# Kernel tuning notes

Hardware: AMD Instinct MI355X
Metric: run time of the kernel (lower is better)

Reference implementation:

```python
import jax, jax.numpy as jnp
import numpy as np
from jax import lax

B, C_IN, H, W = 4, 1536, 24, 24
MID, DIM = 768, 384
HEADS = 8; DIM_HEAD = 48; GROUPS = 8
DS = 3; OFF_SCALE = 4.0; OFF_K = 3
CPB_DIM = DIM // 4  # 96


def conv1x1(x, w):
    # x: (B,Cin,H,W), w: (Cout,Cin)
    return jnp.einsum('bchw,oc->bohw', x, w)


def grouped_conv1x1(x, w):
    # x: (B,G*Ci,H,W), w: (G,Co,Ci)  == torch Conv2d(groups=G, k=1, bias=False)
    b, c, h, ww = x.shape
    g, co, ci = w.shape
    return jnp.einsum('bgihw,goi->bgohw', x.reshape(b, g, ci, h, ww), w).reshape(b, g * co, h, ww)


def grid_sample_bilinear(img, grid):
    # torch F.grid_sample: bilinear, padding_mode='zeros', align_corners=False
    # img (N,C,H,W); grid (N,Ho,Wo,2) with [...,0]=x, [...,1]=y in [-1,1]
    n, c, h, w = img.shape
    x = ((grid[..., 0] + 1.0) * w - 1.0) * 0.5
    y = ((grid[..., 1] + 1.0) * h - 1.0) * 0.5
    x0 = jnp.floor(x); y0 = jnp.floor(y)
    wx = x - x0; wy = y - y0
    x0 = x0.astype(jnp.int32); y0 = y0.astype(jnp.int32)
    img_nhwc = jnp.transpose(img, (0, 2, 3, 1))
    bidx = jnp.arange(n)[:, None, None]

    def tap(ix, iy, wgt):
        valid = (ix >= 0) & (ix < w) & (iy >= 0) & (iy < h)
        v = img_nhwc[bidx, jnp.clip(iy, 0, h - 1), jnp.clip(ix, 0, w - 1)]  # (N,Ho,Wo,C)
        return v * (wgt * valid)[..., None]

    out = (tap(x0, y0, (1 - wx) * (1 - wy)) + tap(x0 + 1, y0, wx * (1 - wy))
           + tap(x0, y0 + 1, (1 - wx) * wy) + tap(x0 + 1, y0 + 1, wx * wy))
    return jnp.transpose(out, (0, 3, 1, 2))


def xy_grid(h, w, dtype):
    # create_grid_like: channel0 = x (width coord), channel1 = y (height coord)
    gx, gy = jnp.meshgrid(jnp.arange(w, dtype=dtype), jnp.arange(h, dtype=dtype), indexing='xy')
    return gx, gy


def normalize_pair(g0, g1, h, w):
    # faithful to lucidrains normalize_grid: channel0 scaled by (h-1), channel1 by (w-1)
    g0 = 2.0 * g0 / max(h - 1, 1) - 1.0
    g1 = 2.0 * g1 / max(w - 1, 1) - 1.0
    return jnp.stack([g0, g1], axis=-1)


def deform_attn(x, Wq, Wk, Wv, Wdw, bdw, Wpw, cw1, cb1, cw2, cb2, cw3, cb3, Wout, bout):
    b, c, h, w = x.shape
    q = grouped_conv1x1(x, Wq)                                 # (b,384,h,w)
    gq = q.reshape(b * GROUPS, c // GROUPS, h, w)
    # to_offsets: depthwise conv k=3 stride=3 pad=0 -> GELU -> 1x1 (->2) -> tanh -> *offset_scale
    off = lax.conv_general_dilated(gq, Wdw, (DS, DS), 'VALID',
                                   dimension_numbers=('NCHW', 'OIHW', 'NCHW'),
                                   feature_group_count=c // GROUPS) + bdw[None, :, None, None]
    off = jax.nn.gelu(off, approximate=False)
    off = jnp.tanh(jnp.einsum('bchw,oc->bohw', off, Wpw)) * OFF_SCALE   # (b*g,2,hp,wp)
    hp, wp = off.shape[-2], off.shape[-1]
    gx, gy = xy_grid(hp, wp, x.dtype)
    vgrid_scaled = normalize_pair(gx + off[:, 0], gy + off[:, 1], hp, wp)  # (b*g,hp,wp,2)
    kv = grid_sample_bilinear(x.reshape(b * GROUPS, c // GROUPS, h, w), vgrid_scaled)
    kv = kv.reshape(b, c, hp, wp)
    k = grouped_conv1x1(kv, Wk); v = grouped_conv1x1(kv, Wv)
    q = q * (DIM_HEAD ** -0.5)
    sh = lambda t: t.reshape(t.shape[0], HEADS, DIM_HEAD, -1).transpose(0, 1, 3, 2)
    qh, kh, vh = sh(q), sh(k), sh(v)                            # (b,H,i,d),(b,H,j,d)
    sim = jnp.einsum('bhid,bhjd->bhij', qh, kh)
    # CPB relative position bias
    qx, qy = xy_grid(h, w, x.dtype)
    grid_q = normalize_pair(qx, qy, h, w).reshape(1, h * w, 2)
    grid_kv = vgrid_scaled.reshape(b * GROUPS, hp * wp, 2)
    pos = grid_q[:, :, None, :] - grid_kv[:, None, :, :]        # (b*g,i,j,2)
    bias = jnp.sign(pos) * jnp.log1p(jnp.abs(pos))
    bias = jax.nn.relu(bias @ cw1.T + cb1)
    bias = jax.nn.relu(bias @ cw2.T + cb2)
    bias = (bias @ cw3.T + cb3).reshape(b, GROUPS, h * w, hp * wp)  # heads//offset_groups == 1
    attn = jax.nn.softmax(sim + bias, axis=-1)
    out = jnp.einsum('bhij,bhjd->bhid', attn, vh)
    out = out.transpose(0, 1, 3, 2).reshape(b, HEADS * DIM_HEAD, h, w)
    return conv1x1(out, Wout) + bout[None, :, None, None]


def setup_inputs() -> dict:
    key = jax.random.key(0)
    ks = jax.random.split(key, 20)
    s = 0.02
    p = lambda i, shape: jax.random.normal(ks[i], shape, jnp.float32) * s
    return {
        'x': jax.random.normal(ks[0], (B, C_IN, H, W), jnp.float32),
        'W1': p(1, (MID, C_IN)), 'W2': p(2, (DIM, MID)),
        'W3': p(3, (MID, DIM)), 'W4': p(4, (C_IN, MID)),
        'Wq': p(5, (GROUPS, DIM // GROUPS, DIM // GROUPS)),
        'Wk': p(6, (GROUPS, DIM // GROUPS, DIM // GROUPS)),
        'Wv': p(7, (GROUPS, DIM // GROUPS, DIM // GROUPS)),
        'Wdw': p(8, (DIM // GROUPS, 1, OFF_K, OFF_K)), 'bdw': p(9, (DIM // GROUPS,)),
        'Wpw': p(10, (2, DIM // GROUPS)),
        'cpb_w1': p(11, (CPB_DIM, 2)), 'cpb_b1': p(12, (CPB_DIM,)),
        'cpb_w2': p(13, (CPB_DIM, CPB_DIM)), 'cpb_b2': p(14, (CPB_DIM,)),
        'cpb_w3': p(15, (1, CPB_DIM)), 'cpb_b3': p(16, (1,)),
        'Wout': p(17, (DIM, DIM)), 'bout': p(18, (DIM,)),
    }


def reference(x, W1, W2, W3, W4, Wq, Wk, Wv, Wdw, bdw, Wpw,
              cpb_w1, cpb_b1, cpb_w2, cpb_b2, cpb_w3, cpb_b3, Wout, bout):
    h = jax.nn.relu(conv1x1(x, W1))
    h = jax.nn.relu(conv1x1(h, W2))
    h = jax.nn.relu(deform_attn(h, Wq, Wk, Wv, Wdw, bdw, Wpw,
                                cpb_w1, cpb_b1, cpb_w2, cpb_b2, cpb_w3, cpb_b3, Wout, bout))
    h = jax.nn.relu(conv1x1(h, W3))
    return jax.nn.relu(conv1x1(h, W4) + x)
```

## Files before the change

### kernel.cpp

```cpp
#include <hip/hip_runtime.h>

typedef float        fx4 __attribute__((ext_vector_type(4)));
typedef float        fx2 __attribute__((ext_vector_type(2)));
typedef unsigned int ux4 __attribute__((ext_vector_type(4)));
typedef short        bf8 __attribute__((ext_vector_type(8)));

#define DEVI static __device__ __forceinline__

DEVI unsigned f2bf1(float f) {
  union { float f; unsigned u; } v; v.f = f;
  return (v.u + 0x7FFFu + ((v.u >> 16) & 1u)) >> 16;
}
DEVI float bf2f(unsigned h) {
  union { unsigned u; float f; } v; v.u = h << 16; return v.f;
}
DEVI unsigned cvtpk(float lo, float hi) {
  unsigned r;
  asm("v_cvt_pk_bf16_f32 %0, %1, %2" : "=v"(r) : "v"(lo), "v"(hi));
  return r;
}
DEVI void unp8(ux4 u, float* o) {
  o[0] = bf2f(u[0] & 0xffffu); o[1] = bf2f(u[0] >> 16);
  o[2] = bf2f(u[1] & 0xffffu); o[3] = bf2f(u[1] >> 16);
  o[4] = bf2f(u[2] & 0xffffu); o[5] = bf2f(u[2] >> 16);
  o[6] = bf2f(u[3] & 0xffffu); o[7] = bf2f(u[3] >> 16);
}
DEVI void gload16(const void* g, void* l) {
  __builtin_amdgcn_global_load_lds(
      (const __attribute__((address_space(1))) unsigned*)(uintptr_t)(g),
      (__attribute__((address_space(3))) unsigned*)(unsigned)(uintptr_t)(l),
      16, 0, 0);
}
#define DPP_ADD(v, ctrl)                                                      \
  do {                                                                        \
    union { float f; int i; } _s, _d;                                         \
    _s.f = (v);                                                               \
    _d.i = __builtin_amdgcn_update_dpp(0, _s.i, (ctrl), 0xf, 0xf, false);     \
    (v) += _d.f;                                                              \
  } while (0)
DEVI float dpp_sum16(float v) {
  DPP_ADD(v, 0xB1);
  DPP_ADD(v, 0x4E);
  DPP_ADD(v, 0x124);
  DPP_ADD(v, 0x128);
  return v;
}

#define TABLO (-1.6f)
#define TABD  (3.2f / 255.f)
#define TABDI (255.f / 3.2f)

__global__ __launch_bounds__(256) void k_wconv(const float* __restrict__ W1,
                                               const float* __restrict__ W2,
                                               const float* __restrict__ W3,
                                               const float* __restrict__ W4,
                                               const float* __restrict__ Wout,
                                               const float* __restrict__ cw2,
                                               const float* __restrict__ Wq,
                                               unsigned* __restrict__ dst,
                                               unsigned* __restrict__ Wqd) {
  const size_t p = (size_t)blockIdx.x * 256 + threadIdx.x;
  if (p < 1552896) {
    const float* s; size_t base;
    if (p < 589824)       { s = W1;   base = 0; }
    else if (p < 737280)  { s = W2;   base = 589824; }
    else if (p < 884736)  { s = W3;   base = 737280; }
    else if (p < 1474560) { s = W4;   base = 884736; }
    else if (p < 1548288) { s = Wout; base = 1474560; }
    else                  { s = cw2;  base = 1548288; }
    const size_t lp = p - base;
    dst[p] = cvtpk(s[lp * 2], s[lp * 2 + 1]);
  } else if (p < 1626624) {
    const int q = (int)(p - 1552896);
    const int o = q / 192, cp = q % 192;
    const int c0 = cp * 2, c1 = c0 + 1;
    const int g = o / 48, lr = o % 48;
    const int lo = g * 48, hi = lo + 48;
    const float f0 = (c0 >= lo && c0 < hi) ? Wq[((size_t)g * 48 + lr) * 48 + (c0 - lo)] : 0.f;
    const float f1 = (c1 >= lo && c1 < hi) ? Wq[((size_t)g * 48 + lr) * 48 + (c1 - lo)] : 0.f;
    Wqd[q] = cvtpk(f0, f1);
  }
}

__global__ __launch_bounds__(256) void k_transpose(const float* __restrict__ x,
                                                   unsigned short* __restrict__ xT) {
  __shared__ float tile[64][65];
  const int t = threadIdx.x;
  const int b = blockIdx.z, c0 = blockIdx.x * 64, p0 = blockIdx.y * 64;
  const int tl = t & 63, th = t >> 6;
#pragma unroll
  for (int r = 0; r < 16; ++r) {
    int c = th * 16 + r;
    tile[c][tl] = x[((size_t)b * 1536 + c0 + c) * 576 + p0 + tl];
  }
  __syncthreads();
#pragma unroll
  for (int r = 0; r < 16; ++r) {
    int p = th * 16 + r;
    xT[((size_t)b * 576 + p0 + p) * 1536 + c0 + tl] = (unsigned short)f2bf1(tile[tl][p]);
  }
}

#define ROWOF(q) ((((q) >> 7) << 4) + ((q) & 15))
#define KOF(q)   (((((q) >> 6) & 1) << 5) + ((((q) >> 4) & 3) << 3))
template<int BN, bool BIASADD, bool FINAL, bool RELU>
__global__ __launch_bounds__(256, 4) void k_gemm(const unsigned short* __restrict__ A,
                                                 const unsigned short* __restrict__ Wb,
                                                 const float* __restrict__ bias,
                                                 const float* __restrict__ resid,
                                                 void* __restrict__ outp, int K, int M) {
  constexpr int BCH = BN / 32;
  constexpr int NJT = BN / 32;
  __shared__ __align__(16) unsigned short As[3][4096];
  __shared__ __align__(16) unsigned short Bs[3][BN * 64];
  const int t = threadIdx.x;
  const int bz = blockIdx.z, j0 = blockIdx.x * BN, i0 = blockIdx.y * 64;
  const int lane = t & 63, wid = t >> 6;
  const int wi = wid >> 1, wj = wid & 1;
  const int lrow = lane & 15, g4 = lane >> 4;

  const unsigned short* pa0 = A + ((size_t)(bz * 576 + i0 + ROWOF(t))) * K + KOF(t);
  const unsigned short* pa1 = A + ((size_t)(bz * 576 + i0 + ROWOF(t + 256))) * K + KOF(t + 256);
  const unsigned short* pb[BCH];
#pragma unroll
  for (int c = 0; c < BCH; ++c) {
    const int q = t + c * 256;
    pb[c] = Wb + ((size_t)(j0 + ROWOF(q))) * K + KOF(q);
  }
  auto stage = [&](int buf, int ko) {
    gload16(pa0 + ko, &As[buf][t * 8]);
    gload16(pa1 + ko, &As[buf][(t + 256) * 8]);
#pragma unroll
    for (int c = 0; c < BCH; ++c) gload16(pb[c] + ko, &Bs[buf][(t + c * 256) * 8]);
  };
  fx4 acc[2][NJT] = {};
  const int nk = K >> 6;
  stage(0, 0);
  if (nk > 1) stage(1, 64);
  int cur = 0;
  for (int ki = 0; ki < nk; ++ki) {
    if (ki + 1 < nk) {
      if constexpr (BCH == 2) asm volatile("s_waitcnt vmcnt(4)" ::: "memory");
      else                    asm volatile("s_waitcnt vmcnt(6)" ::: "memory");
    } else {
      asm volatile("s_waitcnt vmcnt(0)" ::: "memory");
    }
    __builtin_amdgcn_s_barrier();
    __builtin_amdgcn_sched_barrier(0);
    asm volatile("" ::: "memory");
    if (ki + 2 < nk) {
      int b2 = cur - 1; if (b2 < 0) b2 = 2;
      stage(b2, (ki + 2) * 64);
    }
    const unsigned short* ab = &As[cur][0];
    const unsigned short* bb = &Bs[cur][0];
#pragma unroll
    for (int kk = 0; kk < 2; ++kk) {
      bf8 a0 = *(const bf8*)(ab + (((wi * 2 + 0) * 2 + kk) * 64 + lane) * 8);
      bf8 a1 = *(const bf8*)(ab + (((wi * 2 + 1) * 2 + kk) * 64 + lane) * 8);
#pragma unroll
      for (int jt = 0; jt < NJT; ++jt) {
        bf8 b = *(const bf8*)(bb + (((wj * NJT + jt) * 2 + kk) * 64 + lane) * 8);
        acc[0][jt] = __builtin_amdgcn_mfma_f32_16x16x32_bf16(a0, b, acc[0][jt], 0, 0, 0);
        acc[1][jt] = __builtin_amdgcn_mfma_f32_16x16x32_bf16(a1, b, acc[1][jt], 0, 0, 0);
      }
    }
    cur = (cur == 2) ? 0 : cur + 1;
  }
#pragma unroll
  for (int it = 0; it < 2; ++it) {
    const int row0 = i0 + wi * 32 + it * 16 + g4 * 4;
#pragma unroll
    for (int jt = 0; jt < NJT; ++jt) {
      fx4 v = acc[it][jt];
      const int m = j0 + wj * (BN / 2) + jt * 16 + lrow;
      if (BIASADD) {
        float bv = bias[m];
        v[0] += bv; v[1] += bv; v[2] += bv; v[3] += bv;
      }
      if (FINAL) {
        const fx4 xr = *(const fx4*)(resid + ((size_t)bz * M + m) * 576 + row0);
        fx4 ov;
        ov[0] = fmaxf(v[0] + xr[0], 0.f); ov[1] = fmaxf(v[1] + xr[1], 0.f);
        ov[2] = fmaxf(v[2] + xr[2], 0.f); ov[3] = fmaxf(v[3] + xr[3], 0.f);
        *(fx4*)((float*)outp + ((size_t)bz * M + m) * 576 + row0) = ov;
      } else {
        unsigned short* o = (unsigned short*)outp;
#pragma unroll
        for (int r = 0; r < 4; ++r) {
          const float ov = RELU ? fmaxf(v[r], 0.f) : v[r];
          o[((size_t)(bz * 576) + row0 + r) * M + m] = (unsigned short)f2bf1(ov);
        }
      }
    }
  }
}
#undef ROWOF
#undef KOF

__global__ __launch_bounds__(256, 2) void k_sample(const unsigned short* __restrict__ qT,
                                                   const unsigned short* __restrict__ h2T,
                                                   const float* __restrict__ Wdw,
                                                   const float* __restrict__ bdw,
                                                   const float* __restrict__ Wpw,
                                                   const float* __restrict__ Wk,
                                                   const float* __restrict__ Wv,
                                                   float* __restrict__ vgrid,
                                                   float* __restrict__ kT,
                                                   float* __restrict__ vT) {
  __shared__ float vg[32];
  __shared__ __align__(16) unsigned short kvls[768];
  const int blk = blockIdx.x;
  const int bg = blk >> 2, pg = blk & 3;
  const int b = bg >> 3, g = bg & 7;
  const int t = threadIdx.x;
  const int pl = t >> 4;
  const int cq = t & 15;
  const int pos = pg * 16 + pl;
  const int oy = pos >> 3, ox = pos & 7;
  const int ch0 = cq * 3;
  float s0 = bdw[ch0], s1 = bdw[ch0 + 1], s2 = bdw[ch0 + 2];
#pragma unroll
  for (int ky = 0; ky < 3; ++ky) {
#pragma unroll
    for (int kx = 0; kx < 3; ++kx) {
      const unsigned short* rp =
          qT + ((size_t)b * 576 + (oy * 3 + ky) * 24 + ox * 3 + kx) * 384 + g * 48 + ch0;
      const int tap = ky * 3 + kx;
      s0 = fmaf(bf2f(rp[0]), Wdw[(ch0 + 0) * 9 + tap], s0);
      s1 = fmaf(bf2f(rp[1]), Wdw[(ch0 + 1) * 9 + tap], s1);
      s2 = fmaf(bf2f(rp[2]), Wdw[(ch0 + 2) * 9 + tap], s2);
    }
  }
  float a0 = 0.f, a1 = 0.f;
  {
    const float z0 = s0, z1 = s1, z2 = s2;
    const float g0 = 0.5f * z0 * (1.f + erff(z0 * 0.70710678118654752f));
    const float g1 = 0.5f * z1 * (1.f + erff(z1 * 0.70710678118654752f));
    const float g2 = 0.5f * z2 * (1.f + erff(z2 * 0.70710678118654752f));
    a0 = g0 * Wpw[ch0] + g1 * Wpw[ch0 + 1] + g2 * Wpw[ch0 + 2];
    a1 = g0 * Wpw[48 + ch0] + g1 * Wpw[48 + ch0 + 1] + g2 * Wpw[48 + ch0 + 2];
  }
  a0 = dpp_sum16(a0);
  a1 = dpp_sum16(a1);
  const float gx = ((float)ox + tanhf(a0) * 4.f) * (2.f / 7.f) - 1.f;
  const float gy = ((float)oy + tanhf(a1) * 4.f) * (2.f / 7.f) - 1.f;
  if (cq == 0) {
    vg[pl * 2 + 0] = gx; vg[pl * 2 + 1] = gy;
    vgrid[bg * 128 + pos * 2 + 0] = gx;
    vgrid[bg * 128 + pos * 2 + 1] = gy;
  }
  __syncthreads();
  {
    const float nx = vg[pl * 2 + 0], ny = vg[pl * 2 + 1];
    const float xs = ((nx + 1.f) * 24.f - 1.f) * 0.5f;
    const float ys = ((ny + 1.f) * 24.f - 1.f) * 0.5f;
    const float x0f = floorf(xs), y0f = floorf(ys);
    const float wx = xs - x0f, wy = ys - y0f;
    const int x0 = (int)x0f, y0 = (int)y0f;
    float c0a = 0.f, c1a = 0.f, c2a = 0.f;
    const float tw[4] = {(1.f - wx) * (1.f - wy), wx * (1.f - wy), (1.f - wx) * wy, wx * wy};
    const int tx[4] = {x0, x0 + 1, x0, x0 + 1};
    const int ty[4] = {y0, y0, y0 + 1, y0 + 1};
#pragma unroll
    for (int tp = 0; tp < 4; ++tp) {
      const int ix = tx[tp], iy = ty[tp];
      const float w = tw[tp] * ((ix >= 0 && ix < 24 && iy >= 0 && iy < 24) ? 1.f : 0.f);
      const int cx = min(max(ix, 0), 23), cy = min(max(iy, 0), 23);
      const unsigned short* rp = h2T + ((size_t)b * 576 + cy * 24 + cx) * 384 + g * 48 + ch0;
      c0a = fmaf(bf2f(rp[0]), w, c0a);
      c1a = fmaf(bf2f(rp[1]), w, c1a);
      c2a = fmaf(bf2f(rp[2]), w, c2a);
    }
    kvls[pl * 48 + ch0 + 0] = (unsigned short)f2bf1(c0a);
    kvls[pl * 48 + ch0 + 1] = (unsigned short)f2bf1(c1a);
    kvls[pl * 48 + ch0 + 2] = (unsigned short)f2bf1(c2a);
  }
  __syncthreads();
#pragma unroll
  for (int r = 0; r < 3; ++r) {
    const int idx = t + r * 256;
    const int j = idx / 48, o = idx % 48;
    const unsigned short* rp = &kvls[j * 48];
    const float* wkp = Wk + ((size_t)g * 48 + o) * 48;
    const float* wvp = Wv + ((size_t)g * 48 + o) * 48;
    float ak = 0.f, av = 0.f;
#pragma unroll
    for (int c8 = 0; c8 < 6; ++c8) {
      ux4 u = *(const ux4*)(rp + c8 * 8);
      float va[8]; unp8(u, va);
      fx4 wk0 = *(const fx4*)(wkp + c8 * 8); fx4 wk1 = *(const fx4*)(wkp + c8 * 8 + 4);
      fx4 wv0 = *(const fx4*)(wvp + c8 * 8); fx4 wv1 = *(const fx4*)(wvp + c8 * 8 + 4);
#pragma unroll
      for (int e = 0; e < 4; ++e) {
        ak = fmaf(va[e], wk0[e], ak); ak = fmaf(va[4 + e], wk1[e], ak);
        av = fmaf(va[e], wv0[e], av); av = fmaf(va[4 + e], wv1[e], av);
      }
    }
    kT[(size_t)bg * 3072 + (pg * 16 + j) * 48 + o] = ak;
    vT[(size_t)bg * 3072 + (pg * 16 + j) * 48 + o] = av;
  }
}

__global__ __launch_bounds__(256) void k_cpb_tab(const float* __restrict__ cw1,
                                                 const float* __restrict__ cb1,
                                                 const unsigned short* __restrict__ cw2b,
                                                 const float* __restrict__ cb2,
                                                 const float* __restrict__ cw3,
                                                 const float* __restrict__ cb3,
                                                 float* __restrict__ Tb) {
  __shared__ __align__(16) unsigned short Ws[1152 * 8];
  __shared__ __align__(16) float Cs[288];
  const int t = threadIdx.x;
  const int wid = t >> 6, lane = t & 63;
  const int lrow = lane & 15, g16 = lane >> 4;
#pragma unroll
  for (int rep = 0; rep < 5; ++rep) {
    const int q = t + rep * 256;
    if (q < 1152) {
      const int s = q >> 6, l = q & 63;
      const int jt = s / 3, kk = s - jt * 3;
      const int n = jt * 16 + (l & 15);
      const int k = kk * 32 + ((l >> 4) & 3) * 8;
      gload16(cw2b + (size_t)n * 96 + k, &Ws[q * 8]);
    }
  }
  for (int q = t; q < 288; q += 256) Cs[q] = (q < 192) ? cw1[q] : cb1[q - 192];
  float cb2v[6], cw3v[6];
#pragma unroll
  for (int jt = 0; jt < 6; ++jt) {
    cb2v[jt] = cb2[jt * 16 + lrow];
    cw3v[jt] = cw3[jt * 16 + lrow];
  }
  const float cb3v = cb3[0];
  __syncthreads();
  const int base = blockIdx.x * 256 + wid * 64;
  float uu[4], vv[4];
#pragma unroll
  for (int mt = 0; mt < 4; ++mt) {
    const int e = base + mt * 16 + lrow;
    uu[mt] = TABLO + TABD * (float)(e >> 8);
    vv[mt] = TABLO + TABD * (float)(e & 255);
  }
  bf8 afr[4][3];
#pragma unroll
  for (int kk = 0; kk < 3; ++kk) {
    const int kb = kk * 32 + g16 * 8;
    fx4 w0 = *(const fx4*)&Cs[kb * 2];
    fx4 w1 = *(const fx4*)&Cs[kb * 2 + 4];
    fx4 w2 = *(const fx4*)&Cs[kb * 2 + 8];
    fx4 w3 = *(const fx4*)&Cs[kb * 2 + 12];
    fx4 b0 = *(const fx4*)&Cs[192 + kb];
    fx4 b1 = *(const fx4*)&Cs[192 + kb + 4];
#pragma unroll
    for (int mt = 0; mt < 4; ++mt) {
      float h[8];
      h[0] = fmaxf(fmaf(w0[0], uu[mt], fmaf(w0[1], vv[mt], b0[0])), 0.f);
      h[1] = fmaxf(fmaf(w0[2], uu[mt], fmaf(w0[3], vv[mt], b0[1])), 0.f);
      h[2] = fmaxf(fmaf(w1[0], uu[mt], fmaf(w1[1], vv[mt], b0[2])), 0.f);
      h[3] = fmaxf(fmaf(w1[2], uu[mt], fmaf(w1[3], vv[mt], b0[3])), 0.f);
      h[4] = fmaxf(fmaf(w2[0], uu[mt], fmaf(w2[1], vv[mt], b1[0])), 0.f);
      h[5] = fmaxf(fmaf(w2[2], uu[mt], fmaf(w2[3], vv[mt], b1[1])), 0.f);
      h[6] = fmaxf(fmaf(w3[0], uu[mt], fmaf(w3[1], vv[mt], b1[2])), 0.f);
      h[7] = fmaxf(fmaf(w3[2], uu[mt], fmaf(w3[3], vv[mt], b1[3])), 0.f);
      ux4 pk;
      pk[0] = cvtpk(h[0], h[1]); pk[1] = cvtpk(h[2], h[3]);
      pk[2] = cvtpk(h[4], h[5]); pk[3] = cvtpk(h[6], h[7]);
      afr[mt][kk] = *(bf8*)&pk;
    }
  }
  fx4 part[4] = {};
#pragma unroll
  for (int jt = 0; jt < 6; ++jt) {
    bf8 bf0 = *(const bf8*)&Ws[((jt * 3 + 0) * 64 + lane) * 8];
    bf8 bf1 = *(const bf8*)&Ws[((jt * 3 + 1) * 64 + lane) * 8];
    bf8 bf2 = *(const bf8*)&Ws[((jt * 3 + 2) * 64 + lane) * 8];
#pragma unroll
    for (int mt = 0; mt < 4; ++mt) {
      fx4 acc = {cb2v[jt], cb2v[jt], cb2v[jt], cb2v[jt]};
      acc = __builtin_amdgcn_mfma_f32_16x16x32_bf16(afr[mt][0], bf0, acc, 0, 0, 0);
      acc = __builtin_amdgcn_mfma_f32_16x16x32_bf16(afr[mt][1], bf1, acc, 0, 0, 0);
      acc = __builtin_amdgcn_mfma_f32_16x16x32_bf16(afr[mt][2], bf2, acc, 0, 0, 0);
#pragma unroll
      for (int r = 0; r < 4; ++r)
        part[mt][r] = fmaf(fmaxf(acc[r], 0.f), cw3v[jt], part[mt][r]);
    }
  }
#pragma unroll
  for (int mt = 0; mt < 4; ++mt) {
#pragma unroll
    for (int r = 0; r < 4; ++r) part[mt][r] = dpp_sum16(part[mt][r]);
    float pv2 = part[mt][0];
    pv2 = (lrow == 1) ? part[mt][1] : pv2;
    pv2 = (lrow == 2) ? part[mt][2] : pv2;
    pv2 = (lrow == 3) ? part[mt][3] : pv2;
    if (lrow < 4) Tb[base + mt * 16 + g16 * 4 + lrow] = pv2 + cb3v;
  }
}

__global__ __launch_bounds__(256, 3) void k_attn(const unsigned short* __restrict__ qT,
                                                 const float* __restrict__ kT,
                                                 const float* __restrict__ vT,
                                                 const float* __restrict__ vgrid,
                                                 const float* __restrict__ Tb,
                                                 unsigned short* __restrict__ aoT) {
  __shared__ __align__(16) float kls[3072];
  __shared__ __align__(16) float vls[3072];
  __shared__ float vgls[128];
  const int t = threadIdx.x;
  const int ic = blockIdx.x, h = blockIdx.y, b = blockIdx.z;
  const int bg = b * 8 + h;
#pragma unroll
  for (int r = 0; r < 3; ++r) {
    const int idx = t + r * 256;
    ((fx4*)kls)[idx] = ((const fx4*)(kT + (size_t)bg * 3072))[idx];
    ((fx4*)vls)[idx] = ((const fx4*)(vT + (size_t)bg * 3072))[idx];
  }
  if (t < 128) vgls[t] = vgrid[bg * 128 + t];
  __syncthreads();
  const int qi = ic * 64 + (t >> 2);
  const int kg = t & 3;
  const unsigned short* qp = qT + ((size_t)b * 576 + qi) * 384 + h * 48;
  const float scale = 0.14433756729740643f;
  float q[48];
#pragma unroll
  for (int c8 = 0; c8 < 6; ++c8) {
    ux4 u = *(const ux4*)(qp + c8 * 8);
    float va[8]; unp8(u, va);
#pragma unroll
    for (int e = 0; e < 8; ++e) q[c8 * 8 + e] = va[e] * scale;
  }
  float s[16];
  const float* kbase = kls + kg * 16 * 48;
#pragma unroll
  for (int it = 0; it < 16; ++it) {
    const fx4* kr = (const fx4*)(kbase + it * 48);
    float a0 = 0.f, a1 = 0.f;
#pragma unroll
    for (int d4 = 0; d4 < 6; ++d4) {
      fx4 k0 = kr[2 * d4], k1 = kr[2 * d4 + 1];
      a0 = fmaf(q[8 * d4 + 0], k0[0], a0); a0 = fmaf(q[8 * d4 + 1], k0[1], a0);
      a0 = fmaf(q[8 * d4 + 2], k0[2], a0); a0 = fmaf(q[8 * d4 + 3], k0[3], a0);
      a1 = fmaf(q[8 * d4 + 4], k1[0], a1); a1 = fmaf(q[8 * d4 + 5], k1[1], a1);
      a1 = fmaf(q[8 * d4 + 6], k1[2], a1); a1 = fmaf(q[8 * d4 + 7], k1[3], a1);
    }
    s[it] = a0 + a1;
  }
  const float qnx = (float)(qi % 24) * (2.f / 23.f) - 1.f;
  const float qny = (float)(qi / 24) * (2.f / 23.f) - 1.f;
#pragma unroll
  for (int it = 0; it < 16; ++it) {
    const int j = kg * 16 + it;
    const float pu = qnx - vgls[j * 2 + 0];
    const float pv = qny - vgls[j * 2 + 1];
    const float u = copysignf(__logf(1.f + fabsf(pu)), pu);
    const float v = copysignf(__logf(1.f + fabsf(pv)), pv);
    float tu = (u - TABLO) * TABDI;
    float tv = (v - TABLO) * TABDI;
    int iu = (int)floorf(tu); iu = min(max(iu, 0), 254);
    int iv = (int)floorf(tv); iv = min(max(iv, 0), 254);
    const float fu = tu - (float)iu;
    const float fv = tv - (float)iv;
    const float* r0 = Tb + iu * 256 + iv;
    const float a = r0[0], bb2 = r0[1], c = r0[256], d = r0[257];
    const float top = fmaf(fv, bb2 - a, a);
    const float bot = fmaf(fv, d - c, c);
    s[it] += fmaf(fu, bot - top, top);
  }
  float mx = s[0];
#pragma unroll
  for (int it = 1; it < 16; ++it) mx = fmaxf(mx, s[it]);
  mx = fmaxf(mx, __shfl_xor(mx, 1));
  mx = fmaxf(mx, __shfl_xor(mx, 2));
  float sum = 0.f;
#pragma unroll
  for (int it = 0; it < 16; ++it) { s[it] = __expf(s[it] - mx); sum += s[it]; }
  sum += __shfl_xor(sum, 1);
  sum += __shfl_xor(sum, 2);
  const float inv = 1.f / sum;
#pragma unroll
  for (int it = 0; it < 16; ++it) s[it] *= inv;
  float acc[48];
#pragma unroll
  for (int d = 0; d < 48; ++d) acc[d] = 0.f;
  const float* vbase = vls + kg * 16 * 48;
#pragma unroll
  for (int it = 0; it < 16; ++it) {
    const float p = s[it];
    const fx4* vr = (const fx4*)(vbase + it * 48);
#pragma unroll
    for (int d4 = 0; d4 < 12; ++d4) {
      fx4 v = vr[d4];
      acc[d4 * 4 + 0] = fmaf(p, v[0], acc[d4 * 4 + 0]);
      acc[d4 * 4 + 1] = fmaf(p, v[1], acc[d4 * 4 + 1]);
      acc[d4 * 4 + 2] = fmaf(p, v[2], acc[d4 * 4 + 2]);
      acc[d4 * 4 + 3] = fmaf(p, v[3], acc[d4 * 4 + 3]);
    }
  }
#pragma unroll
  for (int d = 0; d < 48; ++d) {
    acc[d] += __shfl_xor(acc[d], 1);
    acc[d] += __shfl_xor(acc[d], 2);
  }
  unsigned* op32 = (unsigned*)(aoT + ((size_t)b * 576 + qi) * 384 + h * 48);
  if (kg == 0) {
#pragma unroll
    for (int p2 = 0; p2 < 6; ++p2) op32[p2] = cvtpk(acc[p2 * 2], acc[p2 * 2 + 1]);
  } else if (kg == 1) {
#pragma unroll
    for (int p2 = 0; p2 < 6; ++p2) op32[6 + p2] = cvtpk(acc[12 + p2 * 2], acc[13 + p2 * 2]);
  } else if (kg == 2) {
#pragma unroll
    for (int p2 = 0; p2 < 6; ++p2) op32[12 + p2] = cvtpk(acc[24 + p2 * 2], acc[25 + p2 * 2]);
  } else {
#pragma unroll
    for (int p2 = 0; p2 < 6; ++p2) op32[18 + p2] = cvtpk(acc[36 + p2 * 2], acc[37 + p2 * 2]);
  }
}

extern "C" void kernel_launch(void* const* d_in, const int* in_sizes, int n_in,
                              void* d_out, int out_size, void* d_ws, size_t ws_size,
                              hipStream_t stream) {
  (void)in_sizes; (void)n_in; (void)out_size; (void)ws_size;
  const float* x    = (const float*)d_in[0];
  const float* W1   = (const float*)d_in[1];
  const float* W2   = (const float*)d_in[2];
  const float* W3   = (const float*)d_in[3];
  const float* W4   = (const float*)d_in[4];
  const float* Wq   = (const float*)d_in[5];
  const float* Wk   = (const float*)d_in[6];
  const float* Wv   = (const float*)d_in[7];
  const float* Wdw  = (const float*)d_in[8];
  const float* bdw  = (const float*)d_in[9];
  const float* Wpw  = (const float*)d_in[10];
  const float* cw1  = (const float*)d_in[11];
  const float* cb1  = (const float*)d_in[12];
  const float* cw2  = (const float*)d_in[13];
  const float* cb2  = (const float*)d_in[14];
  const float* cw3  = (const float*)d_in[15];
  const float* cb3  = (const float*)d_in[16];
  const float* Wout = (const float*)d_in[17];
  const float* bout = (const float*)d_in[18];

  char* ws = (char*)d_ws;
  size_t off = 0;
  auto alloc = [&](size_t bytes) {
    void* p = ws + off;
    off += (bytes + 255) & ~(size_t)255;
    return p;
  };
  unsigned short* xT  = (unsigned short*)alloc((size_t)4 * 576 * 1536 * 2);
  unsigned short* h1T = (unsigned short*)alloc((size_t)4 * 576 * 768 * 2);
  unsigned short* h2T = (unsigned short*)alloc((size_t)4 * 576 * 384 * 2);
  unsigned short* qT  = (unsigned short*)alloc((size_t)4 * 576 * 384 * 2);
  unsigned short* aoT = (unsigned short*)alloc((size_t)4 * 576 * 384 * 2);
  unsigned short* AT  = (unsigned short*)alloc((size_t)4 * 576 * 384 * 2);
  unsigned short* h3T = (unsigned short*)alloc((size_t)4 * 576 * 768 * 2);
  float* vgrid = (float*)alloc((size_t)32 * 64 * 2 * 4);
  float* kTb  = (float*)alloc((size_t)32 * 64 * 48 * 4);
  float* vTb  = (float*)alloc((size_t)32 * 64 * 48 * 4);
  float* Tb    = (float*)alloc((size_t)256 * 256 * 4);
  unsigned short* Wcvt = (unsigned short*)alloc((size_t)3105792 * 2);
  unsigned short* Wqd  = (unsigned short*)alloc((size_t)384 * 384 * 2);
  const unsigned short* W1b   = Wcvt;
  const unsigned short* W2b   = Wcvt + 1179648;
  const unsigned short* W3b   = Wcvt + 1474560;
  const unsigned short* W4b   = Wcvt + 1769472;
  const unsigned short* Woutb = Wcvt + 2949120;
  const unsigned short* cw2b  = Wcvt + 3096576;

  k_wconv<<<6355, 256, 0, stream>>>(W1, W2, W3, W4, Wout, cw2, Wq,
                                    (unsigned*)Wcvt, (unsigned*)Wqd);
  k_cpb_tab<<<256, 256, 0, stream>>>(cw1, cb1, cw2b, cb2, cw3, cb3, Tb);
  k_transpose<<<dim3(24, 9, 4), 256, 0, stream>>>(x, xT);
  k_gemm<64, false, false, true><<<dim3(12, 9, 4), 256, 0, stream>>>(xT, W1b, nullptr, nullptr, h1T, 1536, 768);
  k_gemm<64, false, false, true><<<dim3(6, 9, 4), 256, 0, stream>>>(h1T, W2b, nullptr, nullptr, h2T, 768, 384);
  k_gemm<64, false, false, false><<<dim3(6, 9, 4), 256, 0, stream>>>(h2T, Wqd, nullptr, nullptr, qT, 384, 384);
  k_sample<<<128, 256, 0, stream>>>(qT, h2T, Wdw, bdw, Wpw, Wk, Wv, vgrid, kTb, vTb);
  k_attn<<<dim3(9, 8, 4), 256, 0, stream>>>(qT, kTb, vTb, vgrid, Tb, aoT);
  k_gemm<64, true, false, true><<<dim3(6, 9, 4), 256, 0, stream>>>(aoT, Woutb, bout, nullptr, AT, 384, 384);
  k_gemm<64, false, false, true><<<dim3(12, 9, 4), 256, 0, stream>>>(AT, W3b, nullptr, nullptr, h3T, 384, 768);
  k_gemm<128, false, true, true><<<dim3(12, 9, 4), 256, 0, stream>>>(h3T, W4b, nullptr, x, d_out, 768, 1536);
}
```

Before: 130.4 us.

## Split attention keys across 8 lanes per query with padded LDS rows

Each query in k_attn is now handled by 8 lanes, each owning 8 keys, instead of 4 lanes with 16 keys each, and the grid doubles to 18 blocks along x. Register pressure drops because the 48-float q and acc arrays are replaced by per-chunk 8-float accumulators reduced with DPP/shuffle, and the launch-bounds occupancy hint is removed. K and V rows in LDS are padded to 52 floats with an extra skew every 8 rows to avoid bank conflicts. The cost is that each block reloads the full K/V tile for half as many queries and the output path does more cross-lane reductions.

```diff
diff --git a/kernel.cpp b/kernel.cpp
--- a/kernel.cpp
+++ b/kernel.cpp
@@ -43,6 +43,12 @@
   DPP_ADD(v, 0x4E);
   DPP_ADD(v, 0x124);
   DPP_ADD(v, 0x128);
+  return v;
+}
+DEVI float sum8(float v) {
+  DPP_ADD(v, 0xB1);
+  DPP_ADD(v, 0x4E);
+  v += __shfl_xor(v, 4);
   return v;
 }
 
@@ -398,59 +404,57 @@
   }
 }
 
-__global__ __launch_bounds__(256, 3) void k_attn(const unsigned short* __restrict__ qT,
-                                                 const float* __restrict__ kT,
-                                                 const float* __restrict__ vT,
-                                                 const float* __restrict__ vgrid,
-                                                 const float* __restrict__ Tb,
-                                                 unsigned short* __restrict__ aoT) {
-  __shared__ __align__(16) float kls[3072];
-  __shared__ __align__(16) float vls[3072];
+__global__ __launch_bounds__(256) void k_attn(const unsigned short* __restrict__ qT,
+                                              const float* __restrict__ kT,
+                                              const float* __restrict__ vT,
+                                              const float* __restrict__ vgrid,
+                                              const float* __restrict__ Tb,
+                                              unsigned short* __restrict__ aoT) {
+  __shared__ __align__(16) float kls[3360];
+  __shared__ __align__(16) float vls[3360];
   __shared__ float vgls[128];
   const int t = threadIdx.x;
   const int ic = blockIdx.x, h = blockIdx.y, b = blockIdx.z;
   const int bg = b * 8 + h;
-#pragma unroll
-  for (int r = 0; r < 3; ++r) {
-    const int idx = t + r * 256;
-    ((fx4*)kls)[idx] = ((const fx4*)(kT + (size_t)bg * 3072))[idx];
-    ((fx4*)vls)[idx] = ((const fx4*)(vT + (size_t)bg * 3072))[idx];
+  {
+    const int j = t >> 2, qt = t & 3;
+    const float* sk = kT + (size_t)bg * 3072 + j * 48 + qt * 12;
+    const float* sv = vT + (size_t)bg * 3072 + j * 48 + qt * 12;
+    float* dk = kls + j * 52 + (j >> 3) * 4 + qt * 12;
+    float* dv = vls + j * 52 + (j >> 3) * 4 + qt * 12;
+#pragma unroll
+    for (int e = 0; e < 3; ++e) {
+      ((fx4*)dk)[e] = ((const fx4*)sk)[e];
+      ((fx4*)dv)[e] = ((const fx4*)sv)[e];
+    }
   }
   if (t < 128) vgls[t] = vgrid[bg * 128 + t];
   __syncthreads();
-  const int qi = ic * 64 + (t >> 2);
-  const int kg = t & 3;
+  const int qi = ic * 32 + (t >> 3);
+  const int kg = t & 7;
+  const int rowbase = kg * 420;
   const unsigned short* qp = qT + ((size_t)b * 576 + qi) * 384 + h * 48;
   const float scale = 0.14433756729740643f;
-  float q[48];
+  float s[8] = {0.f, 0.f, 0.f, 0.f, 0.f, 0.f, 0.f, 0.f};
 #pragma unroll
   for (int c8 = 0; c8 < 6; ++c8) {
     ux4 u = *(const ux4*)(qp + c8 * 8);
-    float va[8]; unp8(u, va);
-#pragma unroll
-    for (int e = 0; e < 8; ++e) q[c8 * 8 + e] = va[e] * scale;
-  }
-  float s[16];
-  const float* kbase = kls + kg * 16 * 48;
-#pragma unroll
-  for (int it = 0; it < 16; ++it) {
-    const fx4* kr = (const fx4*)(kbase + it * 48);
-    float a0 = 0.f, a1 = 0.f;
-#pragma unroll
-    for (int d4 = 0; d4 < 6; ++d4) {
-      fx4 k0 = kr[2 * d4], k1 = kr[2 * d4 + 1];
-      a0 = fmaf(q[8 * d4 + 0], k0[0], a0); a0 = fmaf(q[8 * d4 + 1], k0[1], a0);
-      a0 = fmaf(q[8 * d4 + 2], k0[2], a0); a0 = fmaf(q[8 * d4 + 3], k0[3], a0);
-      a1 = fmaf(q[8 * d4 + 4], k1[0], a1); a1 = fmaf(q[8 * d4 + 5], k1[1], a1);
-      a1 = fmaf(q[8 * d4 + 6], k1[2], a1); a1 = fmaf(q[8 * d4 + 7], k1[3], a1);
-    }
-    s[it] = a0 + a1;
+    float qv[8]; unp8(u, qv);
+#pragma unroll
+    for (int it = 0; it < 8; ++it) {
+      const float* kr = kls + rowbase + it * 52 + c8 * 8;
+      fx4 k0 = *(const fx4*)kr, k1 = *(const fx4*)(kr + 4);
+      s[it] = fmaf(qv[0], k0[0], s[it]); s[it] = fmaf(qv[1], k0[1], s[it]);
+      s[it] = fmaf(qv[2], k0[2], s[it]); s[it] = fmaf(qv[3], k0[3], s[it]);
+      s[it] = fmaf(qv[4], k1[0], s[it]); s[it] = fmaf(qv[5], k1[1], s[it]);
+      s[it] = fmaf(qv[6], k1[2], s[it]); s[it] = fmaf(qv[7], k1[3], s[it]);
+    }
   }
   const float qnx = (float)(qi % 24) * (2.f / 23.f) - 1.f;
   const float qny = (float)(qi / 24) * (2.f / 23.f) - 1.f;
 #pragma unroll
-  for (int it = 0; it < 16; ++it) {
-    const int j = kg * 16 + it;
+  for (int it = 0; it < 8; ++it) {
+    const int j = kg * 8 + it;
     const float pu = qnx - vgls[j * 2 + 0];
     const float pv = qny - vgls[j * 2 + 1];
     const float u = copysignf(__logf(1.f + fabsf(pu)), pu);
@@ -465,56 +469,47 @@
     const float a = r0[0], bb2 = r0[1], c = r0[256], d = r0[257];
     const float top = fmaf(fv, bb2 - a, a);
     const float bot = fmaf(fv, d - c, c);
-    s[it] += fmaf(fu, bot - top, top);
+    s[it] = fmaf(s[it], scale, fmaf(fu, bot - top, top));
   }
   float mx = s[0];
 #pragma unroll
-  for (int it = 1; it < 16; ++it) mx = fmaxf(mx, s[it]);
+  for (int it = 1; it < 8; ++it) mx = fmaxf(mx, s[it]);
   mx = fmaxf(mx, __shfl_xor(mx, 1));
   mx = fmaxf(mx, __shfl_xor(mx, 2));
+  mx = fmaxf(mx, __shfl_xor(mx, 4));
   float sum = 0.f;
 #pragma unroll
-  for (int it = 0; it < 16; ++it) { s[it] = __expf(s[it] - mx); sum += s[it]; }
-  sum += __shfl_xor(sum, 1);
-  sum += __shfl_xor(sum, 2);
+  for (int it = 0; it < 8; ++it) { s[it] = __expf(s[it] - mx); sum += s[it]; }
+  sum = sum8(sum);
   const float inv = 1.f / sum;
 #pragma unroll
-  for (int it = 0; it < 16; ++it) s[it] *= inv;
-  float acc[48];
-#pragma unroll
-  for (int d = 0; d < 48; ++d) acc[d] = 0.f;
-  const float* vbase = vls + kg * 16 * 48;
-#pragma unroll
-  for (int it = 0; it < 16; ++it) {
-    const float p = s[it];
-    const fx4* vr = (const fx4*)(vbase + it * 48);
-#pragma unroll
-    for (int d4 = 0; d4 < 12; ++d4) {
-      fx4 v = vr[d4];
-      acc[d4 * 4 + 0] = fmaf(p, v[0], acc[d4 * 4 + 0]);
-      acc[d4 * 4 + 1] = fmaf(p, v[1], acc[d4 * 4 + 1]);
-      acc[d4 * 4 + 2] = fmaf(p, v[2], acc[d4 * 4 + 2]);
-      acc[d4 * 4 + 3] = fmaf(p, v[3], acc[d4 * 4 + 3]);
-    }
-  }
-#pragma unroll
-  for (int d = 0; d < 48; ++d) {
-    acc[d] += __shfl_xor(acc[d], 1);
-    acc[d] += __shfl_xor(acc[d], 2);
-  }
-  unsigned* op32 = (unsigned*)(aoT + ((size_t)b * 576 + qi) * 384 + h * 48);
-  if (kg == 0) {
-#pragma unroll
-    for (int p2 = 0; p2 < 6; ++p2) op32[p2] = cvtpk(acc[p2 * 2], acc[p2 * 2 + 1]);
-  } else if (kg == 1) {
-#pragma unroll
-    for (int p2 = 0; p2 < 6; ++p2) op32[6 + p2] = cvtpk(acc[12 + p2 * 2], acc[13 + p2 * 2]);
-  } else if (kg == 2) {
-#pragma unroll
-    for (int p2 = 0; p2 < 6; ++p2) op32[12 + p2] = cvtpk(acc[24 + p2 * 2], acc[25 + p2 * 2]);
-  } else {
-#pragma unroll
-    for (int p2 = 0; p2 < 6; ++p2) op32[18 + p2] = cvtpk(acc[36 + p2 * 2], acc[37 + p2 * 2]);
+  for (int it = 0; it < 8; ++it) s[it] *= inv;
+  float keep[8];
+#pragma unroll
+  for (int c8 = 0; c8 < 6; ++c8) {
+    float a8[8] = {0.f, 0.f, 0.f, 0.f, 0.f, 0.f, 0.f, 0.f};
+#pragma unroll
+    for (int it = 0; it < 8; ++it) {
+      const float p = s[it];
+      const float* vr = vls + rowbase + it * 52 + c8 * 8;
+      fx4 v0 = *(const fx4*)vr, v1 = *(const fx4*)(vr + 4);
+      a8[0] = fmaf(p, v0[0], a8[0]); a8[1] = fmaf(p, v0[1], a8[1]);
+      a8[2] = fmaf(p, v0[2], a8[2]); a8[3] = fmaf(p, v0[3], a8[3]);
+      a8[4] = fmaf(p, v1[0], a8[4]); a8[5] = fmaf(p, v1[1], a8[5]);
+      a8[6] = fmaf(p, v1[2], a8[6]); a8[7] = fmaf(p, v1[3], a8[7]);
+    }
+#pragma unroll
+    for (int e = 0; e < 8; ++e) {
+      a8[e] = sum8(a8[e]);
+      keep[e] = (kg == c8) ? a8[e] : keep[e];
+    }
+  }
+  if (kg < 6) {
+    unsigned* op32 = (unsigned*)(aoT + ((size_t)b * 576 + qi) * 384 + h * 48 + kg * 8);
+    op32[0] = cvtpk(keep[0], keep[1]);
+    op32[1] = cvtpk(keep[2], keep[3]);
+    op32[2] = cvtpk(keep[4], keep[5]);
+    op32[3] = cvtpk(keep[6], keep[7]);
   }
 }
 
@@ -577,7 +572,7 @@
   k_gemm<64, false, false, true><<<dim3(6, 9, 4), 256, 0, stream>>>(h1T, W2b, nullptr, nullptr, h2T, 768, 384);
   k_gemm<64, false, false, false><<<dim3(6, 9, 4), 256, 0, stream>>>(h2T, Wqd, nullptr, nullptr, qT, 384, 384);
   k_sample<<<128, 256, 0, stream>>>(qT, h2T, Wdw, bdw, Wpw, Wk, Wv, vgrid, kTb, vTb);
-  k_attn<<<dim3(9, 8, 4), 256, 0, stream>>>(qT, kTb, vTb, vgrid, Tb, aoT);
+  k_attn<<<dim3(18, 8, 4), 256, 0, stream>>>(qT, kTb, vTb, vgrid, Tb, aoT);
   k_gemm<64, true, false, true><<<dim3(6, 9, 4), 256, 0, stream>>>(aoT, Woutb, bout, nullptr, AT, 384, 384);
   k_gemm<64, false, false, true><<<dim3(12, 9, 4), 256, 0, stream>>>(AT, W3b, nullptr, nullptr, h3T, 384, 768);
   k_gemm<128, false, true, true><<<dim3(12, 9, 4), 256, 0, stream>>>(h3T, W4b, nullptr, x, d_out, 768, 1536);
```

Measured after the change: 113.5 us. 1.15x faster.
